# Kernel optimization log

Hardware: AMD Instinct MI355X
Metric: run time of the kernel (lower is better)

## Reference

```python
import jax, jax.numpy as jnp
import numpy as np

FRACS = (0.25, 0.5, 0.25)  # per-expert top-fraction kept, from the original forward


def setup_inputs() -> dict:
    key = jax.random.key(0)
    ks = jax.random.split(key, 10)
    B, S, D, P, E, C = 1, 65536, 1024, 512, 3, 2
    s = 0.02
    return {
        "hidden_states": jax.random.normal(ks[0], (B, S, D), jnp.float32),
        "W_t1": jax.random.normal(ks[1], (D, P), jnp.float32) * s,   # TransMIL stand-in proj
        "W_cls1": jax.random.normal(ks[2], (P, C), jnp.float32) * s, # trans1 bag classifier
        "Wg0": jax.random.normal(ks[3], (P, 2), jnp.float32) * s,    # gate
        "Wg1": jax.random.normal(ks[4], (P, 2), jnp.float32) * s,    # gate1
        "Wg2": jax.random.normal(ks[5], (P, 2), jnp.float32) * s,    # gate2
        "W_clf": jax.random.normal(ks[6], (E, P, E), jnp.float32) * s,  # per-expert classifiers
        "W_a1": jax.random.normal(ks[7], (P, P), jnp.float32) * s,   # agg1 TransMIL stand-in proj
        "W_acls": jax.random.normal(ks[8], (P, C), jnp.float32) * s, # agg1 bag classifier
    }


def reference(hidden_states, W_t1, W_cls1, Wg0, Wg1, Wg2, W_clf, W_a1, W_acls):
    B, S, D = hidden_states.shape
    x = hidden_states.reshape(-1, D)               # (T, D) tokens
    T = x.shape[0]
    # trans1 (TransMIL stand-in): per-patch feature + mean-pool bag logits
    patches = jnp.tanh(x @ W_t1)                   # (T, P) patch_feature
    bag = patches.mean(0)
    Y_logits = (bag @ W_cls1)[None, :]             # (1, C)
    Y_prob = jax.nn.softmax(Y_logits, -1)
    Y_hat = jnp.argmax(Y_logits, -1)
    # three independent routers, softmax + top-1
    router_logits = patches @ Wg0                  # (T, 2)
    rw0 = jax.nn.softmax(router_logits.astype(jnp.float32), -1)
    w_top0 = rw0.max(-1)                           # top-1 routing weight (gate0) used as sort key for ALL experts
    sel0 = jnp.argmax(rw0, -1)
    sel1 = jnp.argmax(jax.nn.softmax((patches @ Wg1).astype(jnp.float32), -1), -1)
    sel2 = jnp.argmax(jax.nn.softmax((patches @ Wg2).astype(jnp.float32), -1), -1)
    masks = [sel0 == 1, sel1 == 1, sel2 == 1]      # expert_mask[e][1] token selection
    joint_losses = jnp.float32(0.0)
    sel_fs, nums_list = [], []
    for e in range(3):
        mask = masks[e]
        cnt = mask.sum().astype(jnp.int32)
        nums = jnp.floor(cnt.astype(jnp.float32) * FRACS[e]).astype(jnp.int32)
        nums = jnp.where(nums == 0, cnt, nums)     # 'if nums != 0 else all' branch
        key_ = jnp.where(mask, w_top0, -jnp.inf)
        order = jnp.argsort(-key_)                 # descending routing weight
        rank = jnp.zeros(T, jnp.int32).at[order].set(jnp.arange(T, dtype=jnp.int32))
        sel = mask & (rank < nums)                 # top-fraction tokens of this expert
        sel_f = sel.astype(patches.dtype)
        mean_feat = (patches * sel_f[:, None]).sum(0) / jnp.maximum(nums, 1).astype(patches.dtype)
        logits = mean_feat @ W_clf[e]              # (3,)
        if e < 2:                                  # CE loss only for experts 0,1
            joint_losses = joint_losses + (-jax.nn.log_softmax(logits)[e])
        sel_fs.append(sel_f)
        nums_list.append(nums)
    # agg1 (TransMIL stand-in) over concatenated represent_patchs == multiplicity-weighted mean
    feats2 = jnp.tanh(patches @ W_a1)              # (T, P)
    total_sel = sel_fs[0] + sel_fs[1] + sel_fs[2]
    total_n = (nums_list[0] + nums_list[1] + nums_list[2]).astype(patches.dtype)
    agg_bag = (feats2 * total_sel[:, None]).sum(0) / jnp.maximum(total_n, 1.0)
    e_Y_logits = (agg_bag @ W_acls)[None, :]
    e_Y_hat = jnp.argmax(e_Y_logits, -1)
    distribute = jnp.stack([jnp.asarray(T, jnp.int32), nums_list[0], nums_list[1], nums_list[2]])
    return (e_Y_logits, e_Y_hat, Y_logits, Y_prob, Y_hat, router_logits, joint_losses, distribute)
```

## Files before the change

kernel.cpp:

```cpp
#include <hip/hip_runtime.h>
#include <cstdint>
#include <cstddef>

#define T_TOK 65536
#define DDIM  1024
#define PDIM  512

typedef __attribute__((ext_vector_type(8))) short          shortx8;
typedef __attribute__((ext_vector_type(8))) unsigned short ushortx8;
typedef __attribute__((ext_vector_type(4))) float          floatx4;

__device__ __forceinline__ unsigned short f2bf_rn(float x){
  unsigned int u = __float_as_uint(x);
  unsigned int r = u + 0x7FFFu + ((u >> 16) & 1u);
  return (unsigned short)(r >> 16);
}
__device__ __forceinline__ float bf2f(unsigned short h){
  return __uint_as_float(((unsigned int)h) << 16);
}
__device__ __forceinline__ float ftanh(float x){
  float ez = __expf(2.f * x);
  return 1.f - 2.f / (ez + 1.f);
}

__device__ __forceinline__ void gload16(const void* g, void* l){
  __builtin_amdgcn_global_load_lds(
      (const __attribute__((address_space(1))) unsigned int*)g,
      (__attribute__((address_space(3))) unsigned int*)l, 16, 0, 0);
}
__device__ __forceinline__ void bar(){
  asm volatile("" ::: "memory");
  __builtin_amdgcn_s_barrier();
  asm volatile("" ::: "memory");
}
#define WAIT_VMC(n) asm volatile("s_waitcnt vmcnt(" #n ")" ::: "memory")
#define WAIT_LGKM0  do { asm volatile("s_waitcnt lgkmcnt(0)" ::: "memory"); \
                         __builtin_amdgcn_sched_barrier(0); } while(0)

__device__ __forceinline__ void split2(const float4 a, const float4 b,
                                       ushortx8* hi, ushortx8* lo){
  float vs[8] = {a.x, a.y, a.z, a.w, b.x, b.y, b.z, b.w};
  ushortx8 h, l;
  #pragma unroll
  for (int j = 0; j < 8; j++){
    unsigned int u = __float_as_uint(vs[j]);
    float r = vs[j] - __uint_as_float(u & 0xFFFF0000u);
    h[j] = (unsigned short)(u >> 16);
    l[j] = (unsigned short)(__float_as_uint(r) >> 16);
  }
  *hi = h; *lo = l;
}

__global__ void prep(const float* __restrict__ Wt1, const float* __restrict__ Wa1,
                     unsigned short* __restrict__ W1th, unsigned short* __restrict__ W1tl,
                     unsigned short* __restrict__ Wath, unsigned short* __restrict__ Watl,
                     int* __restrict__ zbase)
{
  int gid = blockIdx.x * 256 + threadIdx.x;
  if (gid < 20544){ zbase[gid] = 0; return; }
  int i = gid - 20544;
  if (i < 524288){
    int e   = i & 7;
    int g16 = i >> 3;
    int s   = g16 & 3;
    int row = (g16 >> 2) & 255;
    int tb  = g16 >> 10;
    int nb  = tb & 1, kt = tb >> 1;
    int n = nb * 256 + row;
    int k = kt * 32 + ((s ^ (row & 3)) << 3) + e;
    float x = Wt1[(size_t)k * PDIM + n];
    unsigned short h = f2bf_rn(x);
    W1th[i] = h;
    W1tl[i] = f2bf_rn(x - bf2f(h));
    return;
  }
  i -= 524288;
  if (i < 262144){
    int e   = i & 7;
    int g16 = i >> 3;
    int s   = g16 & 3;
    int row = (g16 >> 2) & 255;
    int tb  = g16 >> 10;
    int nb  = tb & 1, kt = tb >> 1;
    int n = nb * 256 + row;
    int k = kt * 32 + ((s ^ (row & 3)) << 3) + e;
    float x = Wa1[(size_t)k * PDIM + n];
    unsigned short h = f2bf_rn(x);
    Wath[i] = h;
    Watl[i] = f2bf_rn(x - bf2f(h));
  }
}

template<int MODE>
__global__ __launch_bounds__(512, 2)
void gemm_split(const float* __restrict__ A,
                const unsigned short* __restrict__ Bhg,
                const unsigned short* __restrict__ Blg,
                float* __restrict__ Cout,
                float* __restrict__ colacc,
                const int* __restrict__ cidx,
                const float* __restrict__ wgt,
                const int* __restrict__ params)
{
  constexpr int K  = (MODE == 0) ? 1024 : 512;
  constexpr int NT = K >> 5;

  __shared__ unsigned short AhL[2][8192];
  __shared__ unsigned short AlL[2][8192];
  __shared__ unsigned short BhL[2][8192];
  __shared__ unsigned short BlL[2][8192];
  __shared__ int   cidxl[256];
  __shared__ float wl[256];

  const int tid = threadIdx.x;
  const int d = blockIdx.x + (blockIdx.y << 1);
  const int lin = (MODE == 0) ? (((d & 7) << 6) + (d >> 3)) : d;
  const int bx = lin & 1, by = lin >> 1;
  const int m0 = by << 8, n0 = bx << 8;

  if (MODE == 1){
    const int count = params[21];
    if (m0 >= count) return;
    if (tid < 256){
      int g = m0 + tid;
      if (g < count){ cidxl[tid] = cidx[g]; wl[tid] = wgt[g]; }
      else          { cidxl[tid] = 0;       wl[tid] = 0.f;   }
    }
    __syncthreads();
  }

  const int lane = tid & 63;
  const int wv   = tid >> 6;
  const int wm   = wv >> 2;
  const int wn   = wv & 3;
  const int lr   = lane & 15, quad = lane >> 4;
  const int sq   = (quad ^ (lr & 3)) << 4;

  const int abase = (wm * 128 + lr) * 64 + sq;
  const int bbase = (wn * 64  + lr) * 64 + sq;

  const int rowW = tid >> 1, half = tid & 1;
  const size_t arowg = (MODE == 0) ? (size_t)(m0 + rowW) : (size_t)cidxl[rowW];
  const float* ap = A + arowg * K + half * 16;
  const int wb0 = rowW * 64 + ((( half * 2     ) ^ (rowW & 3)) << 4);
  const int wb1 = rowW * 64 + ((( half * 2 + 1 ) ^ (rowW & 3)) << 4);

  floatx4 acc[8][4];
  #pragma unroll
  for (int i = 0; i < 8; i++)
    #pragma unroll
    for (int j = 0; j < 4; j++)
      acc[i][j] = (floatx4){0.f, 0.f, 0.f, 0.f};

  float4 av0, av1, av2, av3;

  {
    av0 = *(const float4*)(ap + 0);
    av1 = *(const float4*)(ap + 4);
    av2 = *(const float4*)(ap + 8);
    av3 = *(const float4*)(ap + 12);
    const size_t tb = (size_t)bx * 8192;
    gload16(Bhg + tb + tid * 8,        (char*)BhL[0] + tid * 16);
    gload16(Bhg + tb + 4096 + tid * 8, (char*)BhL[0] + 8192 + tid * 16);
    gload16(Blg + tb + tid * 8,        (char*)BlL[0] + tid * 16);
    gload16(Blg + tb + 4096 + tid * 8, (char*)BlL[0] + 8192 + tid * 16);
    WAIT_VMC(4);
    ushortx8 h, l;
    split2(av0, av1, &h, &l);
    *(ushortx8*)((char*)AhL[0] + wb0) = h;
    *(ushortx8*)((char*)AlL[0] + wb0) = l;
    split2(av2, av3, &h, &l);
    *(ushortx8*)((char*)AhL[0] + wb1) = h;
    *(ushortx8*)((char*)AlL[0] + wb1) = l;
    WAIT_VMC(0);
    asm volatile("s_waitcnt lgkmcnt(0)" ::: "memory");
    bar();
  }

  #pragma unroll 2
  for (int t = 0; t < NT; ++t){
    const int cur = t & 1, nxt = cur ^ 1;
    const int kn = (t + 1 < NT) ? (t + 1) : t;
    const char* AhC = (const char*)AhL[cur];
    const char* AlC = (const char*)AlL[cur];
    const char* BhC = (const char*)BhL[cur];
    const char* BlC = (const char*)BlL[cur];

    shortx8 aH[4], aL[4], bH0[2], bL0[2], bH1[2], bL1[2];

    #pragma unroll
    for (int mt = 0; mt < 4; mt++){
      aH[mt] = *(const shortx8*)(AhC + abase + mt * 1024);
      aL[mt] = *(const shortx8*)(AlC + abase + mt * 1024);
    }
    #pragma unroll
    for (int nt = 0; nt < 2; nt++){
      bH0[nt] = *(const shortx8*)(BhC + bbase + nt * 1024);
      bL0[nt] = *(const shortx8*)(BlC + bbase + nt * 1024);
    }
    {
      const float* apk = ap + kn * 32;
      av0 = *(const float4*)(apk);
      av1 = *(const float4*)(apk + 4);
      av2 = *(const float4*)(apk + 8);
      av3 = *(const float4*)(apk + 12);
    }
    bar();
    WAIT_LGKM0;
    __builtin_amdgcn_s_setprio(1);
    #pragma unroll
    for (int mt = 0; mt < 4; mt++)
      #pragma unroll
      for (int nt = 0; nt < 2; nt++){
        acc[mt][nt] = __builtin_amdgcn_mfma_f32_16x16x32_bf16(aH[mt], bH0[nt], acc[mt][nt], 0, 0, 0);
        acc[mt][nt] = __builtin_amdgcn_mfma_f32_16x16x32_bf16(aL[mt], bH0[nt], acc[mt][nt], 0, 0, 0);
        acc[mt][nt] = __builtin_amdgcn_mfma_f32_16x16x32_bf16(aH[mt], bL0[nt], acc[mt][nt], 0, 0, 0);
      }
    __builtin_amdgcn_s_setprio(0);
    bar();

    #pragma unroll
    for (int nt = 0; nt < 2; nt++){
      bH1[nt] = *(const shortx8*)(BhC + bbase + (2 + nt) * 1024);
      bL1[nt] = *(const shortx8*)(BlC + bbase + (2 + nt) * 1024);
    }
    {
      const size_t tb = (size_t)(kn * 2 + bx) * 8192;
      gload16(Bhg + tb + tid * 8,        (char*)BhL[nxt] + tid * 16);
      gload16(Bhg + tb + 4096 + tid * 8, (char*)BhL[nxt] + 8192 + tid * 16);
      gload16(Blg + tb + tid * 8,        (char*)BlL[nxt] + tid * 16);
      gload16(Blg + tb + 4096 + tid * 8, (char*)BlL[nxt] + 8192 + tid * 16);
    }
    bar();
    WAIT_LGKM0;
    __builtin_amdgcn_s_setprio(1);
    #pragma unroll
    for (int mt = 0; mt < 4; mt++)
      #pragma unroll
      for (int nt = 0; nt < 2; nt++){
        acc[mt][2 + nt] = __builtin_amdgcn_mfma_f32_16x16x32_bf16(aH[mt], bH1[nt], acc[mt][2 + nt], 0, 0, 0);
        acc[mt][2 + nt] = __builtin_amdgcn_mfma_f32_16x16x32_bf16(aL[mt], bH1[nt], acc[mt][2 + nt], 0, 0, 0);
        acc[mt][2 + nt] = __builtin_amdgcn_mfma_f32_16x16x32_bf16(aH[mt], bL1[nt], acc[mt][2 + nt], 0, 0, 0);
      }
    __builtin_amdgcn_s_setprio(0);
    bar();

    #pragma unroll
    for (int mt = 0; mt < 4; mt++){
      aH[mt] = *(const shortx8*)(AhC + abase + (4 + mt) * 1024);
      aL[mt] = *(const shortx8*)(AlC + abase + (4 + mt) * 1024);
    }
    WAIT_VMC(4);
    {
      ushortx8 h, l;
      split2(av0, av1, &h, &l);
      *(ushortx8*)((char*)AhL[nxt] + wb0) = h;
      *(ushortx8*)((char*)AlL[nxt] + wb0) = l;
      split2(av2, av3, &h, &l);
      *(ushortx8*)((char*)AhL[nxt] + wb1) = h;
      *(ushortx8*)((char*)AlL[nxt] + wb1) = l;
    }
    bar();
    WAIT_LGKM0;
    __builtin_amdgcn_s_setprio(1);
    #pragma unroll
    for (int mt = 0; mt < 4; mt++)
      #pragma unroll
      for (int nt = 0; nt < 2; nt++){
        acc[4 + mt][nt] = __builtin_amdgcn_mfma_f32_16x16x32_bf16(aH[mt], bH0[nt], acc[4 + mt][nt], 0, 0, 0);
        acc[4 + mt][nt] = __builtin_amdgcn_mfma_f32_16x16x32_bf16(aL[mt], bH0[nt], acc[4 + mt][nt], 0, 0, 0);
        acc[4 + mt][nt] = __builtin_amdgcn_mfma_f32_16x16x32_bf16(aH[mt], bL0[nt], acc[4 + mt][nt], 0, 0, 0);
      }
    __builtin_amdgcn_s_setprio(0);
    bar();

    WAIT_VMC(0);
    bar();
    WAIT_LGKM0;
    __builtin_amdgcn_s_setprio(1);
    #pragma unroll
    for (int mt = 0; mt < 4; mt++)
      #pragma unroll
      for (int nt = 0; nt < 2; nt++){
        acc[4 + mt][2 + nt] = __builtin_amdgcn_mfma_f32_16x16x32_bf16(aH[mt], bH1[nt], acc[4 + mt][2 + nt], 0, 0, 0);
        acc[4 + mt][2 + nt] = __builtin_amdgcn_mfma_f32_16x16x32_bf16(aL[mt], bH1[nt], acc[4 + mt][2 + nt], 0, 0, 0);
        acc[4 + mt][2 + nt] = __builtin_amdgcn_mfma_f32_16x16x32_bf16(aH[mt], bL1[nt], acc[4 + mt][2 + nt], 0, 0, 0);
      }
    __builtin_amdgcn_s_setprio(0);
    bar();
  }

  float csum[4] = {0.f, 0.f, 0.f, 0.f};
  #pragma unroll
  for (int mt = 0; mt < 8; mt++){
    float w0 = 1.f, w1 = 1.f, w2 = 1.f, w3 = 1.f;
    if (MODE == 1){
      const float4 wv4 = *(const float4*)&wl[wm * 128 + mt * 16 + (quad << 2)];
      w0 = wv4.x; w1 = wv4.y; w2 = wv4.z; w3 = wv4.w;
    }
    #pragma unroll
    for (int nt = 0; nt < 4; nt++){
      float t0 = ftanh(acc[mt][nt][0]);
      float t1 = ftanh(acc[mt][nt][1]);
      float t2 = ftanh(acc[mt][nt][2]);
      float t3 = ftanh(acc[mt][nt][3]);
      if (MODE == 0){
        size_t base = (size_t)(m0 + wm * 128 + mt * 16 + (quad << 2)) * PDIM
                    + (n0 + wn * 64 + nt * 16 + lr);
        Cout[base]            = t0;
        Cout[base +     PDIM] = t1;
        Cout[base + 2 * PDIM] = t2;
        Cout[base + 3 * PDIM] = t3;
        csum[nt] += t0 + t1 + t2 + t3;
      } else {
        csum[nt] += t0 * w0 + t1 * w1 + t2 * w2 + t3 * w3;
      }
    }
  }
  #pragma unroll
  for (int nt = 0; nt < 4; nt++){
    float s = csum[nt];
    s += __shfl_xor(s, 16);
    s += __shfl_xor(s, 32);
    if (lane < 16) atomicAdd(&colacc[n0 + wn * 64 + nt * 16 + lane], s);
  }
}

__global__ void gates_kernel(const float* __restrict__ patches,
                             const float* __restrict__ Wg0,
                             const float* __restrict__ Wg1,
                             const float* __restrict__ Wg2,
                             float* __restrict__ dout,
                             unsigned int* __restrict__ wkey,
                             unsigned char* __restrict__ mask3,
                             int* __restrict__ params,
                             int* __restrict__ hist)
{
  __shared__ int lc[3];
  const int tid = threadIdx.x;
  if (tid < 3) lc[tid] = 0;
  __syncthreads();
  const int lane = tid & 63;
  float wg[3][16];
  const float* Wgp[3] = {Wg0, Wg1, Wg2};
  #pragma unroll
  for (int g = 0; g < 3; g++){
    #pragma unroll
    for (int j = 0; j < 4; j++){
      float4 v = *(const float4*)(Wgp[g] + lane * 16 + j * 4);
      wg[g][j * 4 + 0] = v.x; wg[g][j * 4 + 1] = v.y;
      wg[g][j * 4 + 2] = v.z; wg[g][j * 4 + 3] = v.w;
    }
  }
  const int nw = gridDim.x << 2;
  for (int t = blockIdx.x * 4 + (tid >> 6); t < T_TOK; t += nw){
    const float* row = patches + (size_t)t * PDIM + lane * 8;
    float4 v0 = *(const float4*)row;
    float4 v1 = *(const float4*)(row + 4);
    float x[8] = {v0.x, v0.y, v0.z, v0.w, v1.x, v1.y, v1.z, v1.w};
    float g00 = 0, g01 = 0, g10 = 0, g11 = 0, g20 = 0, g21 = 0;
    #pragma unroll
    for (int j = 0; j < 8; j++){
      g00 += x[j] * wg[0][2 * j]; g01 += x[j] * wg[0][2 * j + 1];
      g10 += x[j] * wg[1][2 * j]; g11 += x[j] * wg[1][2 * j + 1];
      g20 += x[j] * wg[2][2 * j]; g21 += x[j] * wg[2][2 * j + 1];
    }
    #pragma unroll
    for (int off = 1; off < 64; off <<= 1){
      g00 += __shfl_xor(g00, off); g01 += __shfl_xor(g01, off);
      g10 += __shfl_xor(g10, off); g11 += __shfl_xor(g11, off);
      g20 += __shfl_xor(g20, off); g21 += __shfl_xor(g21, off);
    }
    if (lane == 0){
      dout[8 + 2 * t]     = g00;
      dout[8 + 2 * t + 1] = g01;
      int m0 = g01 > g00;
      int m1 = g11 > g10;
      int m2 = g21 > g20;
      mask3[t] = (unsigned char)(m0 | (m1 << 1) | (m2 << 2));
      float d = fabsf(g00 - g01);
      float w = 1.0f / (1.0f + __expf(-d));
      unsigned int u = __float_as_uint(w);
      u = u < 0x3F000000u ? 0x3F000000u : u;
      u = u > 0x3F7FFFFFu ? 0x3F7FFFFFu : u;
      wkey[t] = u;
      int b = (int)((u >> 11) & 0xFFFu);
      if (m0){ atomicAdd(&hist[b], 1);         atomicAdd(&lc[0], 1); }
      if (m1){ atomicAdd(&hist[4096 + b], 1);  atomicAdd(&lc[1], 1); }
      if (m2){ atomicAdd(&hist[8192 + b], 1);  atomicAdd(&lc[2], 1); }
    }
  }
  __syncthreads();
  if (tid < 3 && lc[tid]) atomicAdd(&params[tid], lc[tid]);
}

__global__ void find_bucket(int* __restrict__ params, const int* __restrict__ hist)
{
  __shared__ int cs[256], orig[256];
  __shared__ int selc, selrk;
  const int tid = threadIdx.x;
  for (int e = 0; e < 3; e++){
    int cnt = params[e];
    int shift = (e == 1) ? 1 : 2;
    int nums = cnt >> shift;
    if (nums == 0) nums = cnt;
    if (tid == 0) params[3 + e] = nums;
    __syncthreads();
    if (nums == 0){
      if (tid == 0){ params[6 + e] = -1; params[9 + e] = 0; }
      __syncthreads();
      continue;
    }
    const int* h = hist + e * 4096 + tid * 16;
    int s = 0;
    #pragma unroll
    for (int j = 0; j < 16; j++) s += h[j];
    cs[tid] = s; orig[tid] = s;
    __syncthreads();
    for (int off = 1; off < 256; off <<= 1){
      int v = (tid + off < 256) ? cs[tid + off] : 0;
      __syncthreads();
      cs[tid] += v;
      __syncthreads();
    }
    if (cs[tid] >= nums && (cs[tid] - orig[tid]) < nums){
      selc = tid; selrk = nums - (cs[tid] - orig[tid]);
    }
    __syncthreads();
    if (tid == 0){
      int ch = selc, rk = selrk;
      const int* hh = hist + e * 4096 + ch * 16;
      int acc = 0;
      for (int j = 15; j >= 0; j--){
        int c = hh[j];
        if (acc + c >= rk){ params[6 + e] = ch * 16 + j; params[9 + e] = rk - acc; break; }
        acc += c;
      }
    }
    __syncthreads();
  }
}

__global__ void level2hist(const int* __restrict__ params, const unsigned int* __restrict__ wkey,
                           const unsigned char* __restrict__ mask3, int* __restrict__ h2)
{
  const int e = blockIdx.y;
  const int B = params[6 + e];
  if (B < 0) return;
  const unsigned char bit = (unsigned char)(1u << e);
  const int t0 = blockIdx.x * 2048 + threadIdx.x;
  #pragma unroll
  for (int i = 0; i < 8; i++){
    int t = t0 + i * 256;
    if (mask3[t] & bit){
      unsigned int u = wkey[t];
      if ((int)((u >> 11) & 0xFFFu) == B) atomicAdd(&h2[e * 2048 + (u & 2047u)], 1);
    }
  }
}

__global__ void find_theta(int* __restrict__ params, const int* __restrict__ h2)
{
  const int e = blockIdx.x;
  const int tid = threadIdx.x;
  __shared__ int cs[256], orig[256];
  __shared__ int selc;
  int B = params[6 + e], rank = params[9 + e];
  if (B < 0){
    if (tid == 0){ params[12 + e] = (int)0xFFFFFFFFu; params[15 + e] = 0; params[18 + e] = 0; }
    return;
  }
  const int* h = h2 + e * 2048 + tid * 8;
  int s = 0;
  #pragma unroll
  for (int j = 0; j < 8; j++) s += h[j];
  cs[tid] = s; orig[tid] = s;
  __syncthreads();
  for (int off = 1; off < 256; off <<= 1){
    int v = (tid + off < 256) ? cs[tid + off] : 0;
    __syncthreads();
    cs[tid] += v;
    __syncthreads();
  }
  if (cs[tid] >= rank && (cs[tid] - orig[tid]) < rank) selc = tid;
  __syncthreads();
  if (tid == 0){
    int ch = selc;
    int rk = rank - (cs[ch] - orig[ch]);
    const int* hh = h2 + e * 2048 + ch * 8;
    int acc = 0;
    for (int j = 7; j >= 0; j--){
      int c = hh[j];
      if (acc + c >= rk){
        int sub = ch * 8 + j;
        params[12 + e] = (int)(0x3F000000u | ((unsigned)B << 11) | (unsigned)sub);
        params[15 + e] = rk - acc;
        params[18 + e] = c;
        break;
      }
      acc += c;
    }
  }
}

__global__ void mark_sel(const int* __restrict__ params, const unsigned int* __restrict__ wkey,
                         const unsigned char* __restrict__ mask3, unsigned char* __restrict__ selb)
{
  const int e = blockIdx.y;
  const int bx = blockIdx.x;
  const int tid = threadIdx.x;
  const unsigned int theta = (unsigned int)params[12 + e];
  const int r = params[15 + e];
  const int ceq = params[18 + e];
  const unsigned char bit = (unsigned char)(1u << e);
  unsigned char* sb = selb + e * T_TOK;
  if (ceq == r){
    int t0 = bx * 2048;
    #pragma unroll
    for (int i = 0; i < 8; i++){
      int t = t0 + i * 256 + tid;
      unsigned char mk = mask3[t] & bit;
      sb[t] = (mk && wkey[t] >= theta) ? 1 : 0;
    }
  } else {
    if (bx) return;
    __shared__ int basec;
    __shared__ int wsum[4];
    if (tid == 0) basec = 0;
    __syncthreads();
    const int lane = tid & 63, w = tid >> 6;
    for (int c = 0; c < 256; c++){
      int t = c * 256 + tid;
      unsigned char mk = mask3[t] & bit;
      unsigned int u = mk ? wkey[t] : 0u;
      bool gt = mk && (u > theta);
      bool eq = mk && (u == theta);
      unsigned long long bal = __ballot(eq);
      if (lane == 0) wsum[w] = __popcll(bal);
      __syncthreads();
      int wbase = 0;
      for (int ww = 0; ww < w; ww++) wbase += wsum[ww];
      int pos = basec + wbase + __popcll(bal & ((1ull << lane) - 1ull));
      sb[t] = (gt || (eq && pos < r)) ? 1 : 0;
      __syncthreads();
      if (tid == 0) basec += wsum[0] + wsum[1] + wsum[2] + wsum[3];
      __syncthreads();
    }
  }
}

__global__ void compact(const unsigned char* __restrict__ selb, int* __restrict__ cidx,
                        float* __restrict__ wgt, int* __restrict__ params)
{
  int t = blockIdx.x * 256 + threadIdx.x;
  int ts = selb[t] + selb[T_TOK + t] + selb[2 * T_TOK + t];
  int lane = threadIdx.x & 63;
  unsigned long long bal = __ballot(ts > 0);
  int base = 0;
  if (lane == 0) base = atomicAdd(&params[21], __popcll(bal));
  base = __shfl(base, 0);
  if (ts){
    int pos = base + __popcll(bal & ((1ull << lane) - 1ull));
    cidx[pos] = t;
    wgt[pos] = (float)ts;
  }
}

__global__ void meanfeat_c(const float* __restrict__ patches, const unsigned char* __restrict__ selb,
                           const int* __restrict__ cidx, const int* __restrict__ params,
                           float* __restrict__ mf)
{
  const int count = params[21];
  const int base = blockIdx.x * 256;
  if (base >= count) return;
  const int n = min(256, count - base);
  const int tid = threadIdx.x;
  __shared__ int cl[256];
  __shared__ unsigned char f0s[256], f1s[256];
  if (tid < n){
    int c = cidx[base + tid];
    cl[tid] = c;
    f0s[tid] = selb[c];
    f1s[tid] = selb[T_TOK + c];
  }
  __syncthreads();
  float s00 = 0, s01 = 0, s10 = 0, s11 = 0;
  for (int i = 0; i < n; i++){
    int f0 = f0s[i], f1 = f1s[i];
    if (f0 | f1){
      float2 v = *(const float2*)(patches + (size_t)cl[i] * PDIM + tid * 2);
      if (f0){ s00 += v.x; s01 += v.y; }
      if (f1){ s10 += v.x; s11 += v.y; }
    }
  }
  atomicAdd(&mf[tid * 2],       s00);
  atomicAdd(&mf[tid * 2 + 1],   s01);
  atomicAdd(&mf[512 + tid * 2],     s10);
  atomicAdd(&mf[512 + tid * 2 + 1], s11);
}

__global__ void finalize(const float* __restrict__ bagsum, const float* __restrict__ aggsum,
                         const float* __restrict__ mf, const int* __restrict__ params,
                         const float* __restrict__ Wcls1, const float* __restrict__ Wclf,
                         const float* __restrict__ Wacls, float* __restrict__ dout)
{
  const int lane = threadIdx.x;
  const int nums0 = params[3], nums1 = params[4], nums2 = params[5];
  const float invT = 1.0f / 65536.0f;
  const float inv0 = 1.0f / (float)(nums0 > 0 ? nums0 : 1);
  const float inv1 = 1.0f / (float)(nums1 > 0 ? nums1 : 1);
  const float totn = (float)(nums0 + nums1 + nums2);
  const float invA = 1.0f / fmaxf(totn, 1.0f);
  float y0 = 0, y1 = 0, a0 = 0, a1 = 0;
  float l00 = 0, l01 = 0, l02 = 0, l10 = 0, l11 = 0, l12 = 0;
  #pragma unroll
  for (int j = 0; j < 8; j++){
    int p = lane * 8 + j;
    float bg = bagsum[p] * invT;
    y0 += bg * Wcls1[p * 2]; y1 += bg * Wcls1[p * 2 + 1];
    float ag = aggsum[p] * invA;
    a0 += ag * Wacls[p * 2]; a1 += ag * Wacls[p * 2 + 1];
    float m0v = mf[p] * inv0;
    l00 += m0v * Wclf[p * 3]; l01 += m0v * Wclf[p * 3 + 1]; l02 += m0v * Wclf[p * 3 + 2];
    float m1v = mf[512 + p] * inv1;
    l10 += m1v * Wclf[1536 + p * 3]; l11 += m1v * Wclf[1536 + p * 3 + 1]; l12 += m1v * Wclf[1536 + p * 3 + 2];
  }
  #pragma unroll
  for (int off = 1; off < 64; off <<= 1){
    y0 += __shfl_xor(y0, off);   y1 += __shfl_xor(y1, off);
    a0 += __shfl_xor(a0, off);   a1 += __shfl_xor(a1, off);
    l00 += __shfl_xor(l00, off); l01 += __shfl_xor(l01, off); l02 += __shfl_xor(l02, off);
    l10 += __shfl_xor(l10, off); l11 += __shfl_xor(l11, off); l12 += __shfl_xor(l12, off);
  }
  if (lane == 0){
    dout[0] = a0; dout[1] = a1;
    dout[2] = (a1 > a0) ? 1.0f : 0.0f;
    dout[3] = y0; dout[4] = y1;
    float mx = fmaxf(y0, y1), e0 = expf(y0 - mx), e1 = expf(y1 - mx), inv = 1.0f / (e0 + e1);
    dout[5] = e0 * inv; dout[6] = e1 * inv;
    dout[7] = (y1 > y0) ? 1.0f : 0.0f;
    float m3 = fmaxf(fmaxf(l00, l01), l02);
    float lse0 = m3 + logf(expf(l00 - m3) + expf(l01 - m3) + expf(l02 - m3));
    float m4 = fmaxf(fmaxf(l10, l11), l12);
    float lse1 = m4 + logf(expf(l10 - m4) + expf(l11 - m4) + expf(l12 - m4));
    dout[131080] = (lse0 - l00) + (lse1 - l11);
    dout[131081] = 65536.0f;
    dout[131082] = (float)nums0;
    dout[131083] = (float)nums1;
    dout[131084] = (float)nums2;
  }
}

extern "C" void kernel_launch(void* const* d_in, const int* in_sizes, int n_in,
                              void* d_out, int out_size, void* d_ws, size_t ws_size,
                              hipStream_t stream)
{
  const float* X      = (const float*)d_in[0];
  const float* W_t1   = (const float*)d_in[1];
  const float* W_cls1 = (const float*)d_in[2];
  const float* Wg0    = (const float*)d_in[3];
  const float* Wg1    = (const float*)d_in[4];
  const float* Wg2    = (const float*)d_in[5];
  const float* W_clf  = (const float*)d_in[6];
  const float* W_a1   = (const float*)d_in[7];
  const float* W_acls = (const float*)d_in[8];
  float* dout = (float*)d_out;
  char* ws = (char*)d_ws;

  float*          patches = (float*)         (ws + 0);
  unsigned short* W1th    = (unsigned short*)(ws + 134217728);
  unsigned short* W1tl    = (unsigned short*)(ws + 135266304);
  unsigned short* Wath    = (unsigned short*)(ws + 136314880);
  unsigned short* Watl    = (unsigned short*)(ws + 136839168);
  unsigned int*   wkey    = (unsigned int*)  (ws + 137363456);
  unsigned char*  mask3   = (unsigned char*) (ws + 137625600);
  unsigned char*  selb    = (unsigned char*) (ws + 137691136);
  int*            cidx    = (int*)           (ws + 137887744);
  float*          wgt     = (float*)         (ws + 138149888);
  int*            zbase   = (int*)           (ws + 138412032);
  int*            hist    = zbase;
  int*            h2      = zbase + 12288;
  int*            params  = zbase + 18432;
  float*          bagsum  = (float*)(zbase + 18496);
  float*          aggsum  = (float*)(zbase + 19008);
  float*          mf      = (float*)(zbase + 19520);

  prep<<<3153, 256, 0, stream>>>(W_t1, W_a1, W1th, W1tl, Wath, Watl, zbase);

  gemm_split<0><<<dim3(2, 256), 512, 0, stream>>>(
      X, W1th, W1tl, patches, bagsum, nullptr, nullptr, nullptr);

  gates_kernel<<<512, 256, 0, stream>>>(
      patches, Wg0, Wg1, Wg2, dout, wkey, mask3, params, hist);

  find_bucket<<<1, 256, 0, stream>>>(params, hist);
  level2hist<<<dim3(32, 3), 256, 0, stream>>>(params, wkey, mask3, h2);
  find_theta<<<3, 256, 0, stream>>>(params, h2);
  mark_sel<<<dim3(32, 3), 256, 0, stream>>>(params, wkey, mask3, selb);
  compact<<<256, 256, 0, stream>>>(selb, cidx, wgt, params);

  meanfeat_c<<<256, 256, 0, stream>>>(patches, selb, cidx, params, mf);

  gemm_split<1><<<dim3(2, 256), 512, 0, stream>>>(
      patches, Wath, Watl, nullptr, aggsum, cidx, wgt, params);

  finalize<<<1, 64, 0, stream>>>(bagsum, aggsum, mf, params, W_cls1, W_clf, W_acls, dout);
}
```

Measured before the change: 765.8 us.

## Deepen A prefetch pipeline, reorder B loads, and change LDS swizzle

Global loads of the fp32 A tile are now issued two k-steps ahead, while the next B tiles are issued at the start of each iteration. The hi/lo split of A into LDS moves earlier. The last two MFMA phases are merged, removing one barrier and the full vmcnt(0) drain per iteration. The LDS XOR swizzle now uses (row>>1)&3 instead of row&3, applied consistently in both the prep layout and the kernel reads and writes, to cut bank conflicts. This costs more register pressure and relies on tighter ordering of the vmcnt waits.

```diff
diff --git a/kernel.cpp b/kernel.cpp
--- a/kernel.cpp
+++ b/kernel.cpp
@@ -50,6 +50,7 @@
   }
   *hi = h; *lo = l;
 }
+
 
 __global__ void prep(const float* __restrict__ Wt1, const float* __restrict__ Wa1,
                      unsigned short* __restrict__ W1th, unsigned short* __restrict__ W1tl,
@@ -67,7 +68,7 @@
     int tb  = g16 >> 10;
     int nb  = tb & 1, kt = tb >> 1;
     int n = nb * 256 + row;
-    int k = kt * 32 + ((s ^ (row & 3)) << 3) + e;
+    int k = kt * 32 + ((s ^ ((row >> 1) & 3)) << 3) + e;
     float x = Wt1[(size_t)k * PDIM + n];
     unsigned short h = f2bf_rn(x);
     W1th[i] = h;
@@ -83,7 +84,7 @@
     int tb  = g16 >> 10;
     int nb  = tb & 1, kt = tb >> 1;
     int n = nb * 256 + row;
-    int k = kt * 32 + ((s ^ (row & 3)) << 3) + e;
+    int k = kt * 32 + ((s ^ ((row >> 1) & 3)) << 3) + e;
     float x = Wa1[(size_t)k * PDIM + n];
     unsigned short h = f2bf_rn(x);
     Wath[i] = h;
@@ -134,7 +135,7 @@
   const int wm   = wv >> 2;
   const int wn   = wv & 3;
   const int lr   = lane & 15, quad = lane >> 4;
-  const int sq   = (quad ^ (lr & 3)) << 4;
+  const int sq   = (quad ^ ((lr >> 1) & 3)) << 4;
 
   const int abase = (wm * 128 + lr) * 64 + sq;
   const int bbase = (wn * 64  + lr) * 64 + sq;
@@ -142,8 +143,9 @@
   const int rowW = tid >> 1, half = tid & 1;
   const size_t arowg = (MODE == 0) ? (size_t)(m0 + rowW) : (size_t)cidxl[rowW];
   const float* ap = A + arowg * K + half * 16;
-  const int wb0 = rowW * 64 + ((( half * 2     ) ^ (rowW & 3)) << 4);
-  const int wb1 = rowW * 64 + ((( half * 2 + 1 ) ^ (rowW & 3)) << 4);
+  const int rsw = (rowW >> 1) & 3;
+  const int wb0 = rowW * 64 + ((( half * 2     ) ^ rsw) << 4);
+  const int wb1 = rowW * 64 + ((( half * 2 + 1 ) ^ rsw) << 4);
 
   floatx4 acc[8][4];
   #pragma unroll
@@ -172,7 +174,14 @@
     split2(av2, av3, &h, &l);
     *(ushortx8*)((char*)AhL[0] + wb1) = h;
     *(ushortx8*)((char*)AlL[0] + wb1) = l;
-    WAIT_VMC(0);
+    {
+      const float* apk = ap + ((NT > 1) ? 32 : 0);
+      av0 = *(const float4*)(apk);
+      av1 = *(const float4*)(apk + 4);
+      av2 = *(const float4*)(apk + 8);
+      av3 = *(const float4*)(apk + 12);
+    }
+    WAIT_VMC(4);
     asm volatile("s_waitcnt lgkmcnt(0)" ::: "memory");
     bar();
   }
@@ -180,7 +189,8 @@
   #pragma unroll 2
   for (int t = 0; t < NT; ++t){
     const int cur = t & 1, nxt = cur ^ 1;
-    const int kn = (t + 1 < NT) ? (t + 1) : t;
+    const int knB = (t + 1 < NT) ? (t + 1) : (NT - 1);
+    const int knA = (t + 2 < NT) ? (t + 2) : (NT - 1);
     const char* AhC = (const char*)AhL[cur];
     const char* AlC = (const char*)AlL[cur];
     const char* BhC = (const char*)BhL[cur];
@@ -199,11 +209,11 @@
       bL0[nt] = *(const shortx8*)(BlC + bbase + nt * 1024);
     }
     {
-      const float* apk = ap + kn * 32;
-      av0 = *(const float4*)(apk);
-      av1 = *(const float4*)(apk + 4);
-      av2 = *(const float4*)(apk + 8);
-      av3 = *(const float4*)(apk + 12);
+      const size_t tb = (size_t)(knB * 2 + bx) * 8192;
+      gload16(Bhg + tb + tid * 8,        (char*)BhL[nxt] + tid * 16);
+      gload16(Bhg + tb + 4096 + tid * 8, (char*)BhL[nxt] + 8192 + tid * 16);
+      gload16(Blg + tb + tid * 8,        (char*)BlL[nxt] + tid * 16);
+      gload16(Blg + tb + 4096 + tid * 8, (char*)BlL[nxt] + 8192 + tid * 16);
     }
     bar();
     WAIT_LGKM0;
@@ -224,12 +234,15 @@
       bH1[nt] = *(const shortx8*)(BhC + bbase + (2 + nt) * 1024);
       bL1[nt] = *(const shortx8*)(BlC + bbase + (2 + nt) * 1024);
     }
+    WAIT_VMC(4);
     {
-      const size_t tb = (size_t)(kn * 2 + bx) * 8192;
-      gload16(Bhg + tb + tid * 8,        (char*)BhL[nxt] + tid * 16);
-      gload16(Bhg + tb + 4096 + tid * 8, (char*)BhL[nxt] + 8192 + tid * 16);
-      gload16(Blg + tb + tid * 8,        (char*)BlL[nxt] + tid * 16);
-      gload16(Blg + tb + 4096 + tid * 8, (char*)BlL[nxt] + 8192 + tid * 16);
+      ushortx8 h, l;
+      split2(av0, av1, &h, &l);
+      *(ushortx8*)((char*)AhL[nxt] + wb0) = h;
+      *(ushortx8*)((char*)AlL[nxt] + wb0) = l;
+      split2(av2, av3, &h, &l);
+      *(ushortx8*)((char*)AhL[nxt] + wb1) = h;
+      *(ushortx8*)((char*)AlL[nxt] + wb1) = l;
     }
     bar();
     WAIT_LGKM0;
@@ -250,15 +263,12 @@
       aH[mt] = *(const shortx8*)(AhC + abase + (4 + mt) * 1024);
       aL[mt] = *(const shortx8*)(AlC + abase + (4 + mt) * 1024);
     }
-    WAIT_VMC(4);
     {
-      ushortx8 h, l;
-      split2(av0, av1, &h, &l);
-      *(ushortx8*)((char*)AhL[nxt] + wb0) = h;
-      *(ushortx8*)((char*)AlL[nxt] + wb0) = l;
-      split2(av2, av3, &h, &l);
-      *(ushortx8*)((char*)AhL[nxt] + wb1) = h;
-      *(ushortx8*)((char*)AlL[nxt] + wb1) = l;
+      const float* apk = ap + knA * 32;
+      av0 = *(const float4*)(apk);
+      av1 = *(const float4*)(apk + 4);
+      av2 = *(const float4*)(apk + 8);
+      av3 = *(const float4*)(apk + 12);
     }
     bar();
     WAIT_LGKM0;
@@ -271,13 +281,6 @@
         acc[4 + mt][nt] = __builtin_amdgcn_mfma_f32_16x16x32_bf16(aL[mt], bH0[nt], acc[4 + mt][nt], 0, 0, 0);
         acc[4 + mt][nt] = __builtin_amdgcn_mfma_f32_16x16x32_bf16(aH[mt], bL0[nt], acc[4 + mt][nt], 0, 0, 0);
       }
-    __builtin_amdgcn_s_setprio(0);
-    bar();
-
-    WAIT_VMC(0);
-    bar();
-    WAIT_LGKM0;
-    __builtin_amdgcn_s_setprio(1);
     #pragma unroll
     for (int mt = 0; mt < 4; mt++)
       #pragma unroll
@@ -287,6 +290,7 @@
         acc[4 + mt][2 + nt] = __builtin_amdgcn_mfma_f32_16x16x32_bf16(aH[mt], bL1[nt], acc[4 + mt][2 + nt], 0, 0, 0);
       }
     __builtin_amdgcn_s_setprio(0);
+    WAIT_VMC(4);
     bar();
   }
 
```

New measurement: 726.6 us. 1.05x faster.
